# Kernel optimization log

Hardware: AMD Instinct MI355X
Metric: run time of the kernel (lower is better)

Reference implementation:

```python
import jax, jax.numpy as jnp
import numpy as np

# Topologies derived from init kwargs (inputs=64, outputs=64, state=512, net1 hidden=[512])
D = 64 + 64 + 512                      # 640 = concat(input, prev_output, state)
NET1 = [D, 512, 64]
NET3 = [D] + NET1 + [512]              # [640, 640, 512, 64, 512] (code reuses mutated net1 topo)
W_TOTAL = sum(NET3[j] * NET3[j + 1] for j in range(len(NET3) - 1))  # 802816
B_TOTAL = sum(NET3[1:])                # 1728
NET2 = [D] + NET1 + [W_TOTAL + B_TOTAL]  # [640, 640, 512, 64, 804544]


def _leaky(v):
    return jnp.where(v >= 0, v, 0.01 * v)


def setup_inputs() -> dict:
    key = jax.random.key(0)
    ks = jax.random.split(key, 16)
    inp = {
        "x": jax.random.normal(ks[0], (64,), jnp.float32),
        "prev_output": jnp.zeros((64,), jnp.float32),
        "state": jnp.zeros((512,), jnp.float32),
    }
    # net1 params (Linear stores W as [out, in])
    for i in range(len(NET1) - 1):
        inp[f"net1_w{i}"] = jax.random.normal(ks[1 + i], (NET1[i + 1], NET1[i]), jnp.float32) * 0.02
        inp[f"net1_b{i}"] = jnp.zeros((NET1[i + 1],), jnp.float32)
    # net2 params
    for i in range(len(NET2) - 1):
        inp[f"net2_w{i}"] = jax.random.normal(ks[5 + i], (NET2[i + 1], NET2[i]), jnp.float32) * 0.02
        inp[f"net2_b{i}"] = jnp.zeros((NET2[i + 1],), jnp.float32)
    return inp


def reference(x, prev_output, state,
              net1_w0, net1_b0, net1_w1, net1_b1,
              net2_w0, net2_b0, net2_w1, net2_b1,
              net2_w2, net2_b2, net2_w3, net2_b3):
    inpt = jnp.concatenate([x, prev_output, state])  # [640]

    # net2: hypernetwork producing flattened weights+biases for net3
    h = _leaky(net2_w0 @ inpt + net2_b0)
    h = _leaky(net2_w1 @ h + net2_b1)
    h = _leaky(net2_w2 @ h + net2_b2)
    x2 = jnp.tanh(net2_w3 @ h + net2_b3) * 0.5       # [W_TOTAL + B_TOTAL]
    weights = x2[:W_TOTAL]
    bias = x2[W_TOTAL:]

    # net3: apply generated weights sequentially (state update)
    x3 = inpt
    wi, bi = 0, 0
    for j in range(1, len(NET3)):
        out_d, in_d = NET3[j], NET3[j - 1]
        W = weights[wi:wi + out_d * in_d].reshape(out_d, in_d)
        b = bias[bi:bi + out_d]
        x3 = W @ x3 + b                               # 1D: x3 @ W.T == W @ x3
        if j != len(NET3) - 1:
            x3 = _leaky(x3)
        wi += out_d * in_d
        bi += out_d
    new_state = x3                                    # [512]

    # net1: output head
    h1 = _leaky(net1_w0 @ inpt + net1_b0)
    out = net1_w1 @ h1 + net1_b1                      # [64]

    # torch forward returns only `out`; new_state is the persistent buffer
    # update. We concatenate both so the full step math is observable.
    return jnp.concatenate([out, new_state])          # [576]
```

## Files before the change

kernel.cpp:

```cpp
#include <hip/hip_runtime.h>
#include <math.h>


#define WS_H0    0
#define WS_H1N1  640
#define WS_H1N2  1152
#define WS_H2    1664
#define WS_INPT  1728
#define WS_X3A   2368
#define WS_X3B   3008
#define WS_X3C   3520

__device__ __forceinline__ float leaky_f(float v) { return v >= 0.0f ? v : 0.01f * v; }

__device__ __forceinline__ float uni(float v) {
  return __int_as_float(__builtin_amdgcn_readfirstlane(__float_as_int(v)));
}

__device__ __forceinline__ float inpt_at(int i, const float* x, const float* po, const float* st) {
  return i < 64 ? x[i] : (i < 128 ? po[i - 64] : st[i - 128]);
}

__device__ __forceinline__ float x2val(const float* __restrict__ w3, const float* __restrict__ b3,
                                       long long r, const float* hs) {
  const float4* row = (const float4*)(w3 + (r << 6));
  float d0 = 0.f, d1 = 0.f, d2 = 0.f, d3 = 0.f;
#pragma unroll
  for (int k = 0; k < 16; k++) {
    float4 v = row[k];
    d0 = fmaf(v.x, hs[4 * k + 0], d0);
    d1 = fmaf(v.y, hs[4 * k + 1], d1);
    d2 = fmaf(v.z, hs[4 * k + 2], d2);
    d3 = fmaf(v.w, hs[4 * k + 3], d3);
  }
  float d = ((d0 + d1) + (d2 + d3)) + b3[r];
  float t = exp2f(d * 2.8853900817779268f);
  return 0.5f - __builtin_amdgcn_rcpf(t + 1.0f);
}

__device__ __forceinline__ void load_h_uniform(const float* __restrict__ h2p, float* hs) {
  const float4* h4 = (const float4*)h2p;
#pragma unroll
  for (int k = 0; k < 16; k++) {
    float4 v = h4[k];
    hs[4 * k + 0] = uni(v.x);
    hs[4 * k + 1] = uni(v.y);
    hs[4 * k + 2] = uni(v.z);
    hs[4 * k + 3] = uni(v.w);
  }
}

template <int IN>
__device__ __forceinline__ float row_dot(const float* __restrict__ wrow, const float* s_in, int lane) {
  const float4* w4 = (const float4*)wrow;
  const float4* s4 = (const float4*)s_in;
  float acc = 0.f;
  for (int j = lane; j < IN / 4; j += 64) {
    float4 a = w4[j];
    float4 b = s4[j];
    acc += a.x * b.x + a.y * b.y + a.z * b.z + a.w * b.w;
  }
  for (int off = 32; off; off >>= 1) acc += __shfl_xor(acc, off, 64);
  return acc;
}

__global__ __launch_bounds__(256) void k1a(const float* __restrict__ x, const float* __restrict__ po,
                                           const float* __restrict__ st,
                                           const float* __restrict__ w2_0, const float* __restrict__ b2_0,
                                           const float* __restrict__ w1_0, const float* __restrict__ b1_0,
                                           float* __restrict__ ws) {
  __shared__ __align__(16) float s_in[640];
  for (int i = threadIdx.x; i < 640; i += 256) {
    float v = inpt_at(i, x, po, st);
    s_in[i] = v;
    ws[WS_INPT + i] = v;
  }
  __syncthreads();
  int wave = threadIdx.x >> 6, lane = threadIdx.x & 63;
  int o = blockIdx.x * 4 + wave;
  const float* wrow;
  float bias;
  float* dst;
  if (o < 640) {
    wrow = w2_0 + (long long)o * 640; bias = b2_0[o]; dst = ws + WS_H0 + o;
  } else {
    int oo = o - 640;
    wrow = w1_0 + (long long)oo * 640; bias = b1_0[oo]; dst = ws + WS_H1N1 + oo;
  }
  float acc = row_dot<640>(wrow, s_in, lane);
  if (lane == 0) *dst = leaky_f(acc + bias);
}

__global__ __launch_bounds__(256) void k1b(const float* __restrict__ w2_1, const float* __restrict__ b2_1,
                                           const float* __restrict__ w1_1, const float* __restrict__ b1_1,
                                           float* __restrict__ ws, float* __restrict__ out) {
  __shared__ __align__(16) float s_h0[640];
  __shared__ __align__(16) float s_h1[512];
  for (int i = threadIdx.x; i < 640; i += 256) s_h0[i] = ws[WS_H0 + i];
  for (int i = threadIdx.x; i < 512; i += 256) s_h1[i] = ws[WS_H1N1 + i];
  __syncthreads();
  int wave = threadIdx.x >> 6, lane = threadIdx.x & 63;
  int o = blockIdx.x * 4 + wave;
  if (o < 512) {
    float acc = row_dot<640>(w2_1 + (long long)o * 640, s_h0, lane);
    if (lane == 0) ws[WS_H1N2 + o] = leaky_f(acc + b2_1[o]);
  } else {
    int oo = o - 512;
    float acc = row_dot<512>(w1_1 + (long long)oo * 512, s_h1, lane);
    if (lane == 0) out[oo] = acc + b1_1[oo];
  }
}

__global__ __launch_bounds__(256) void k1c(const float* __restrict__ w2_2, const float* __restrict__ b2_2,
                                           float* __restrict__ ws) {
  __shared__ __align__(16) float s_h[512];
  for (int i = threadIdx.x; i < 512; i += 256) s_h[i] = ws[WS_H1N2 + i];
  __syncthreads();
  int wave = threadIdx.x >> 6, lane = threadIdx.x & 63;
  int o = blockIdx.x * 4 + wave;
  float acc = row_dot<512>(w2_2 + (long long)o * 512, s_h, lane);
  if (lane == 0) ws[WS_H2 + o] = leaky_f(acc + b2_2[o]);
}

template <int IN_D, bool LEAKY>
__global__ __launch_bounds__(512) void k2(const float* __restrict__ w3, const float* __restrict__ b3,
                                          const float* __restrict__ h2p, const float* __restrict__ x3in,
                                          float* __restrict__ x3out, long long wi, long long brow) {
  __shared__ __align__(16) float s_in[IN_D];
  __shared__ float s_red[8];
  float hs[64];
  load_h_uniform(h2p, hs);
  for (int i = threadIdx.x; i < IN_D; i += 512) s_in[i] = x3in[i];
  __syncthreads();

  int o = blockIdx.x;
  float acc = 0.0f;
  for (int i = threadIdx.x; i < IN_D; i += 512) {
    long long r = wi + (long long)o * IN_D + i;
    acc += x2val(w3, b3, r, hs) * s_in[i];
  }
  if (threadIdx.x == 511) acc += x2val(w3, b3, brow + o, hs);

  for (int off = 32; off; off >>= 1) acc += __shfl_xor(acc, off, 64);
  int wave = threadIdx.x >> 6, lane = threadIdx.x & 63;
  if (lane == 0) s_red[wave] = acc;
  __syncthreads();
  if (threadIdx.x == 0) {
    float tot = 0.f;
#pragma unroll
    for (int w = 0; w < 8; w++) tot += s_red[w];
    x3out[o] = LEAKY ? leaky_f(tot) : tot;
  }
}

__global__ __launch_bounds__(256) void k2d(const float* __restrict__ w3, const float* __restrict__ b3,
                                           const float* __restrict__ ws, float* __restrict__ out) {
  float hs[64];
  load_h_uniform(ws + WS_H2, hs);
  int wave = threadIdx.x >> 6, lane = threadIdx.x & 63;
  int o = blockIdx.x * 4 + wave;
  long long r = 770048LL + (long long)o * 64 + lane;
  float acc = x2val(w3, b3, r, hs) * ws[WS_X3C + lane];
  if (lane == 0) acc += x2val(w3, b3, 804032LL + o, hs);
  for (int off = 32; off; off >>= 1) acc += __shfl_xor(acc, off, 64);
  if (lane == 0) out[64 + o] = acc;
}

extern "C" void kernel_launch(void* const* d_in, const int* in_sizes, int n_in,
                              void* d_out, int out_size, void* d_ws, size_t ws_size,
                              hipStream_t stream) {
  const float* x    = (const float*)d_in[0];
  const float* po   = (const float*)d_in[1];
  const float* st   = (const float*)d_in[2];
  const float* w1_0 = (const float*)d_in[3];
  const float* b1_0 = (const float*)d_in[4];
  const float* w1_1 = (const float*)d_in[5];
  const float* b1_1 = (const float*)d_in[6];
  const float* w2_0 = (const float*)d_in[7];
  const float* b2_0 = (const float*)d_in[8];
  const float* w2_1 = (const float*)d_in[9];
  const float* b2_1 = (const float*)d_in[10];
  const float* w2_2 = (const float*)d_in[11];
  const float* b2_2 = (const float*)d_in[12];
  const float* w3   = (const float*)d_in[13];
  const float* b3   = (const float*)d_in[14];
  float* ws  = (float*)d_ws;
  float* out = (float*)d_out;

  k1a<<<288, 256, 0, stream>>>(x, po, st, w2_0, b2_0, w1_0, b1_0, ws);
  k1b<<<144, 256, 0, stream>>>(w2_1, b2_1, w1_1, b1_1, ws, out);
  k1c<<<16, 256, 0, stream>>>(w2_2, b2_2, ws);
  k2<640, true><<<640, 512, 0, stream>>>(w3, b3, ws + WS_H2, ws + WS_INPT, ws + WS_X3A, 0LL, 802816LL);
  k2<640, true><<<512, 512, 0, stream>>>(w3, b3, ws + WS_H2, ws + WS_X3A, ws + WS_X3B, 409600LL, 803456LL);
  k2<512, true><<<64, 512, 0, stream>>>(w3, b3, ws + WS_H2, ws + WS_X3B, ws + WS_X3C, 737280LL, 803968LL);
  k2d<<<128, 256, 0, stream>>>(w3, b3, ws, out);
}
```

Before: 351.3 us.

## Compute hypernetwork rows with 16-lane cooperative coalesced loads instead of per-thread rows

Replaces the per-thread 64-wide dot product over a generated weight row with a scheme where 16 lanes each load one float4 of the row and combine partials through shuffle reductions. Each wave instruction then reads contiguous memory, which should improve coalescing and cut the 64-register h array and its per-thread strided reads. The last layer now reuses the same templated kernel with IN_D=64 in place of the separate k2d kernel. In exchange it adds shuffle reduction work and leaves 15 of every 16 lanes idle during the accumulation step.

```diff
diff --git a/kernel.cpp b/kernel.cpp
--- a/kernel.cpp
+++ b/kernel.cpp
@@ -13,41 +13,13 @@
 
 __device__ __forceinline__ float leaky_f(float v) { return v >= 0.0f ? v : 0.01f * v; }
 
-__device__ __forceinline__ float uni(float v) {
-  return __int_as_float(__builtin_amdgcn_readfirstlane(__float_as_int(v)));
-}
-
 __device__ __forceinline__ float inpt_at(int i, const float* x, const float* po, const float* st) {
   return i < 64 ? x[i] : (i < 128 ? po[i - 64] : st[i - 128]);
 }
 
-__device__ __forceinline__ float x2val(const float* __restrict__ w3, const float* __restrict__ b3,
-                                       long long r, const float* hs) {
-  const float4* row = (const float4*)(w3 + (r << 6));
-  float d0 = 0.f, d1 = 0.f, d2 = 0.f, d3 = 0.f;
-#pragma unroll
-  for (int k = 0; k < 16; k++) {
-    float4 v = row[k];
-    d0 = fmaf(v.x, hs[4 * k + 0], d0);
-    d1 = fmaf(v.y, hs[4 * k + 1], d1);
-    d2 = fmaf(v.z, hs[4 * k + 2], d2);
-    d3 = fmaf(v.w, hs[4 * k + 3], d3);
-  }
-  float d = ((d0 + d1) + (d2 + d3)) + b3[r];
+__device__ __forceinline__ float half_tanh(float d) {
   float t = exp2f(d * 2.8853900817779268f);
   return 0.5f - __builtin_amdgcn_rcpf(t + 1.0f);
-}
-
-__device__ __forceinline__ void load_h_uniform(const float* __restrict__ h2p, float* hs) {
-  const float4* h4 = (const float4*)h2p;
-#pragma unroll
-  for (int k = 0; k < 16; k++) {
-    float4 v = h4[k];
-    hs[4 * k + 0] = uni(v.x);
-    hs[4 * k + 1] = uni(v.y);
-    hs[4 * k + 2] = uni(v.z);
-    hs[4 * k + 3] = uni(v.w);
-  }
 }
 
 template <int IN>
@@ -123,47 +95,58 @@
 }
 
 template <int IN_D, bool LEAKY>
-__global__ __launch_bounds__(512) void k2(const float* __restrict__ w3, const float* __restrict__ b3,
-                                          const float* __restrict__ h2p, const float* __restrict__ x3in,
-                                          float* __restrict__ x3out, long long wi, long long brow) {
+__global__ __launch_bounds__(512) void k2c(const float* __restrict__ w3, const float* __restrict__ b3,
+                                           const float* __restrict__ h2p, const float* __restrict__ x3in,
+                                           float* __restrict__ x3out, long long wi, long long brow) {
   __shared__ __align__(16) float s_in[IN_D];
   __shared__ float s_red[8];
-  float hs[64];
-  load_h_uniform(h2p, hs);
-  for (int i = threadIdx.x; i < IN_D; i += 512) s_in[i] = x3in[i];
+  const int tid = threadIdx.x;
+  const int wave = tid >> 6, lane = tid & 63;
+  const int g = lane >> 4;
+  const int gl = lane & 15;
+
+  float4 hv = ((const float4*)h2p)[gl];
+  for (int i = tid; i < IN_D; i += 512) s_in[i] = x3in[i];
   __syncthreads();
 
-  int o = blockIdx.x;
+  const int o = blockIdx.x;
+  const long long rowbase = wi + (long long)o * IN_D;
   float acc = 0.0f;
-  for (int i = threadIdx.x; i < IN_D; i += 512) {
-    long long r = wi + (long long)o * IN_D + i;
-    acc += x2val(w3, b3, r, hs) * s_in[i];
+  constexpr int STEPS = IN_D / 32;
+#pragma unroll
+  for (int s = 0; s < STEPS; s++) {
+    int rl = s * 32 + wave * 4 + g;
+    long long r = rowbase + rl;
+    float4 v = ((const float4*)(w3 + (r << 6)))[gl];
+    float d = v.x * hv.x + v.y * hv.y + v.z * hv.z + v.w * hv.w;
+    d += __shfl_xor(d, 1, 64);
+    d += __shfl_xor(d, 2, 64);
+    d += __shfl_xor(d, 4, 64);
+    d += __shfl_xor(d, 8, 64);
+    d += b3[r];
+    float x2v = half_tanh(d);
+    if (gl == 0) acc += x2v * s_in[rl];
   }
-  if (threadIdx.x == 511) acc += x2val(w3, b3, brow + o, hs);
-
+  if (wave == 0 && lane < 16) {
+    long long rb = brow + o;
+    float4 v = ((const float4*)(w3 + (rb << 6)))[gl];
+    float d = v.x * hv.x + v.y * hv.y + v.z * hv.z + v.w * hv.w;
+    d += __shfl_xor(d, 1, 64);
+    d += __shfl_xor(d, 2, 64);
+    d += __shfl_xor(d, 4, 64);
+    d += __shfl_xor(d, 8, 64);
+    d += b3[rb];
+    if (lane == 0) acc += half_tanh(d);
+  }
   for (int off = 32; off; off >>= 1) acc += __shfl_xor(acc, off, 64);
-  int wave = threadIdx.x >> 6, lane = threadIdx.x & 63;
   if (lane == 0) s_red[wave] = acc;
   __syncthreads();
-  if (threadIdx.x == 0) {
+  if (tid == 0) {
     float tot = 0.f;
 #pragma unroll
     for (int w = 0; w < 8; w++) tot += s_red[w];
     x3out[o] = LEAKY ? leaky_f(tot) : tot;
   }
-}
-
-__global__ __launch_bounds__(256) void k2d(const float* __restrict__ w3, const float* __restrict__ b3,
-                                           const float* __restrict__ ws, float* __restrict__ out) {
-  float hs[64];
-  load_h_uniform(ws + WS_H2, hs);
-  int wave = threadIdx.x >> 6, lane = threadIdx.x & 63;
-  int o = blockIdx.x * 4 + wave;
-  long long r = 770048LL + (long long)o * 64 + lane;
-  float acc = x2val(w3, b3, r, hs) * ws[WS_X3C + lane];
-  if (lane == 0) acc += x2val(w3, b3, 804032LL + o, hs);
-  for (int off = 32; off; off >>= 1) acc += __shfl_xor(acc, off, 64);
-  if (lane == 0) out[64 + o] = acc;
 }
 
 extern "C" void kernel_launch(void* const* d_in, const int* in_sizes, int n_in,
@@ -190,8 +173,8 @@
   k1a<<<288, 256, 0, stream>>>(x, po, st, w2_0, b2_0, w1_0, b1_0, ws);
   k1b<<<144, 256, 0, stream>>>(w2_1, b2_1, w1_1, b1_1, ws, out);
   k1c<<<16, 256, 0, stream>>>(w2_2, b2_2, ws);
-  k2<640, true><<<640, 512, 0, stream>>>(w3, b3, ws + WS_H2, ws + WS_INPT, ws + WS_X3A, 0LL, 802816LL);
-  k2<640, true><<<512, 512, 0, stream>>>(w3, b3, ws + WS_H2, ws + WS_X3A, ws + WS_X3B, 409600LL, 803456LL);
-  k2<512, true><<<64, 512, 0, stream>>>(w3, b3, ws + WS_H2, ws + WS_X3B, ws + WS_X3C, 737280LL, 803968LL);
-  k2d<<<128, 256, 0, stream>>>(w3, b3, ws, out);
+  k2c<640, true><<<640, 512, 0, stream>>>(w3, b3, ws + WS_H2, ws + WS_INPT, ws + WS_X3A, 0LL, 802816LL);
+  k2c<640, true><<<512, 512, 0, stream>>>(w3, b3, ws + WS_H2, ws + WS_X3A, ws + WS_X3B, 409600LL, 803456LL);
+  k2c<512, true><<<64, 512, 0, stream>>>(w3, b3, ws + WS_H2, ws + WS_X3B, ws + WS_X3C, 737280LL, 803968LL);
+  k2c<64, false><<<512, 512, 0, stream>>>(w3, b3, ws + WS_H2, ws + WS_X3C, out + 64, 770048LL, 804032LL);
 }
```

Measured after the change: 355.6 us. No clear change (+1.2%).
